# Performance work log

Hardware: AMD Instinct MI355X
Metric: run time of the kernel (lower is better)

The kernel has to match this reference:

```python
import jax, jax.numpy as jnp
import numpy as np

M = 16                      # multiplicity of each irrep block
INV3 = 1.0 / np.sqrt(3.0)   # w3j(1,1,0) component-normalized
INV2 = 1.0 / np.sqrt(2.0)   # w3j(1,1,1) component-normalized
A0 = 1.0 / np.sqrt(2.0 * M) # fan-in norm for 0e outputs (2 paths x mul 16)
A1 = 1.0 / np.sqrt(3.0 * M) # fan-in norm for 1o outputs (3 paths x mul 16)


def setup_inputs() -> dict:
    E, N, ED, HID = 100000, 10000, 32, 128
    WNUM = 2 * M * (2 * M) + 3 * M * M  # 1792 per-edge TP weights
    ks = jax.random.split(jax.random.key(0), 10)
    return {
        "dst": jax.random.randint(ks[0], (E,), 0, N),
        "x_src": jax.random.normal(ks[1], (E, 4 * M), jnp.float32),   # 16x0e+16x1o
        "x_dst": jax.random.normal(ks[2], (N, 4 * M), jnp.float32),
        "sh": jax.random.normal(ks[3], (E, 4), jnp.float32),          # 1x0e+1x1o
        "edge_attr": jax.random.normal(ks[4], (E, ED), jnp.float32),
        "We1": jax.random.normal(ks[5], (ED, HID), jnp.float32) / np.sqrt(ED),
        "be1": jnp.zeros((HID,), jnp.float32),
        "We2": jax.random.normal(ks[6], (HID, WNUM), jnp.float32) / np.sqrt(HID),
        "be2": jnp.zeros((WNUM,), jnp.float32),
        "Wr0": jax.random.normal(ks[7], (M, 2 * M), jnp.float32),     # 16x0e -> 32x0e
        "Wr1": jax.random.normal(ks[8], (M, M), jnp.float32),         # 16x1o -> 16x1o
    }


def _forward(dst, x_src, x_dst, sh, edge_attr, We1, be1, We2, be2, Wr0, Wr1):
    E = x_src.shape[0]
    N = x_dst.shape[0]
    o0 = 2 * M  # 32x0e tp output (scalars + gates)

    # edge MLP -> per-edge tensor-product weights [E, 1792]
    w = jax.nn.relu(edge_attr @ We1 + be1) @ We2 + be2
    i = 0
    w_ss = w[:, i:i + M * o0].reshape(E, M, o0); i += M * o0   # 0e x 0e -> 0e
    w_vv0 = w[:, i:i + M * o0].reshape(E, M, o0); i += M * o0  # 1o x 1o -> 0e
    w_sv = w[:, i:i + M * M].reshape(E, M, M); i += M * M      # 0e x 1o -> 1o
    w_vs = w[:, i:i + M * M].reshape(E, M, M); i += M * M      # 1o x 0e -> 1o
    w_vv1 = w[:, i:i + M * M].reshape(E, M, M)                 # 1o x 1o -> 1o

    s1 = x_src[:, :M]                       # [E, 16]
    v1 = x_src[:, M:].reshape(E, M, 3)      # [E, 16, 3]
    s2 = sh[:, 0]                           # [E]
    v2 = sh[:, 1:4]                         # [E, 3]

    # fully-connected tensor product with per-edge weights
    out0 = A0 * (jnp.einsum('em,emo->eo', s1 * s2[:, None], w_ss)
                 + INV3 * jnp.einsum('emc,ec,emo->eo', v1, v2, w_vv0))  # [E, 32]
    cross = jnp.cross(v1, v2[:, None, :])   # [E, 16, 3]
    out1 = A1 * (jnp.einsum('em,ec,emo->eoc', s1, v2, w_sv)
                 + jnp.einsum('emc,e,emo->eoc', v1, s2, w_vs)
                 + INV2 * jnp.einsum('emc,emo->eoc', cross, w_vv1))     # [E, 16, 3]
    msg = jnp.concatenate([out0, out1.reshape(E, -1)], axis=1)          # [E, 80]

    # scatter-mean over destination nodes
    ssum = jax.ops.segment_sum(msg, dst, num_segments=N)
    cnt = jax.ops.segment_sum(jnp.ones((E,), msg.dtype), dst, num_segments=N)
    msg = ssum / jnp.maximum(cnt, 1.0)[:, None]                          # [N, 80]

    # residual equivariant linear on x_dst
    sd = x_dst[:, :M]
    vd = x_dst[:, M:].reshape(N, M, 3)
    res0 = (sd @ Wr0) / np.sqrt(M)                                       # [N, 32]
    res1 = jnp.einsum('nmc,mo->noc', vd, Wr1) / np.sqrt(M)               # [N, 16, 3]
    msg = msg + jnp.concatenate([res0, res1.reshape(N, -1)], axis=1)

    # gate nonlinearity: relu(scalars), sigmoid(gates) * gated vectors
    scalars = jax.nn.relu(msg[:, :M])
    gates = jax.nn.sigmoid(msg[:, M:2 * M])
    gated = msg[:, 2 * M:].reshape(N, M, 3) * gates[:, :, None]
    return jnp.concatenate([scalars, gated.reshape(N, -1)], axis=1)      # [N, 64]


def reference(dst, x_src, x_dst, sh, edge_attr, We1, be1, We2, be2, Wr0, Wr1):
    return _forward(dst, x_src, x_dst, sh, edge_attr, We1, be1, We2, be2, Wr0, Wr1)
```

## Files before the change

### kernel.cpp

```cpp
#include <hip/hip_runtime.h>
#include <math.h>

#define WNUM 1792
#define HID 128

#define INV3C 0.5773502691896258f
#define INV2C 0.7071067811865476f
#define A0C   0.17677669529663687f
#define A1C   0.14433756729740643f
#define MAXDEG 64

typedef short bf8 __attribute__((ext_vector_type(8)));
typedef _Float16 f16x8 __attribute__((ext_vector_type(8)));
typedef _Float16 f16x4 __attribute__((ext_vector_type(4)));
typedef float f32x4 __attribute__((ext_vector_type(4)));

__device__ inline unsigned short f2bf(float f) {
  union { float f; unsigned u; } v; v.f = f;
  unsigned r = v.u + 0x7FFFu + ((v.u >> 16) & 1u);
  return (unsigned short)(r >> 16);
}
__device__ inline float bf2f(unsigned short h) {
  union { unsigned u; float f; } v; v.u = ((unsigned)h) << 16;
  return v.f;
}
__device__ inline float wscale(int t) {
  if (t < 32) return A0C;
  if (t < 64) return A0C * INV3C;
  if (t < 96) return A1C;
  return A1C * INV2C;
}

__global__ __launch_bounds__(256) void prep_kernel(
    const float* __restrict__ We1, const float* __restrict__ We2,
    const float* __restrict__ be2,
    unsigned short* __restrict__ we1x, _Float16* __restrict__ we2h,
    float* __restrict__ be2p, int* __restrict__ cntp, int N)
{
  int i = blockIdx.x * 256 + threadIdx.x;
  if (i < 28672) {
    int t = i >> 8, c = (i >> 6) & 3, lane = i & 63;
    int quad = lane >> 4, l15 = lane & 15;
    int col = t * 16 + l15;
    float sc = wscale(t);
    f16x8 v;
    #pragma unroll
    for (int j = 0; j < 8; ++j) {
      int k = c * 32 + quad * 8 + j;
      v[j] = (_Float16)(We2[(size_t)k * WNUM + col] * sc);
    }
    *(f16x8*)(we2h + (size_t)t * 2048 + c * 512 + lane * 8) = v;
  } else if (i < 29184) {
    int q = i - 28672;
    int c1 = q >> 6, lane = q & 63;
    int quad = lane >> 4, l15 = lane & 15;
    int col = c1 * 16 + l15;
    bf8 hh, ll;
    #pragma unroll
    for (int j = 0; j < 8; ++j) {
      int k = quad * 8 + j;
      float v = We1[k * HID + col];
      unsigned short hi = f2bf(v);
      hh[j] = (short)hi;
      ll[j] = (short)f2bf(v - bf2f(hi));
    }
    *(bf8*)(we1x + c1 * 1024 + lane * 8) = hh;
    *(bf8*)(we1x + c1 * 1024 + 512 + lane * 8) = ll;
  } else if (i < 30976) {
    int q = i - 29184;
    int t = q >> 4, l16 = q & 15;
    be2p[(t >> 1) * 32 + l16 * 2 + (t & 1)] = be2[q] * wscale(t);
  } else if (i < 30976 + N) {
    cntp[i - 30976] = 0;
  }
}

__device__ inline void chains2(const f16x8* a0, const f16x8* a1,
    f16x8 b0, f16x8 b1, f16x8 b2, f16x8 b3,
    f16x8 b4, f16x8 b5, f16x8 b6, f16x8 b7,
    float2 bias, f32x4* wa, f32x4* wb)
{
  f32x4 ca0 = {bias.x, bias.x, bias.x, bias.x};
  f32x4 cb0 = {bias.y, bias.y, bias.y, bias.y};
  f32x4 ca1 = ca0, cb1 = cb0;
  ca0 = __builtin_amdgcn_mfma_f32_16x16x32_f16(a0[0], b0, ca0, 0, 0, 0);
  cb0 = __builtin_amdgcn_mfma_f32_16x16x32_f16(a0[0], b4, cb0, 0, 0, 0);
  ca1 = __builtin_amdgcn_mfma_f32_16x16x32_f16(a1[0], b0, ca1, 0, 0, 0);
  cb1 = __builtin_amdgcn_mfma_f32_16x16x32_f16(a1[0], b4, cb1, 0, 0, 0);
  ca0 = __builtin_amdgcn_mfma_f32_16x16x32_f16(a0[1], b1, ca0, 0, 0, 0);
  cb0 = __builtin_amdgcn_mfma_f32_16x16x32_f16(a0[1], b5, cb0, 0, 0, 0);
  ca1 = __builtin_amdgcn_mfma_f32_16x16x32_f16(a1[1], b1, ca1, 0, 0, 0);
  cb1 = __builtin_amdgcn_mfma_f32_16x16x32_f16(a1[1], b5, cb1, 0, 0, 0);
  ca0 = __builtin_amdgcn_mfma_f32_16x16x32_f16(a0[2], b2, ca0, 0, 0, 0);
  cb0 = __builtin_amdgcn_mfma_f32_16x16x32_f16(a0[2], b6, cb0, 0, 0, 0);
  ca1 = __builtin_amdgcn_mfma_f32_16x16x32_f16(a1[2], b2, ca1, 0, 0, 0);
  cb1 = __builtin_amdgcn_mfma_f32_16x16x32_f16(a1[2], b6, cb1, 0, 0, 0);
  ca0 = __builtin_amdgcn_mfma_f32_16x16x32_f16(a0[3], b3, ca0, 0, 0, 0);
  cb0 = __builtin_amdgcn_mfma_f32_16x16x32_f16(a0[3], b7, cb0, 0, 0, 0);
  ca1 = __builtin_amdgcn_mfma_f32_16x16x32_f16(a1[3], b3, ca1, 0, 0, 0);
  cb1 = __builtin_amdgcn_mfma_f32_16x16x32_f16(a1[3], b7, cb1, 0, 0, 0);
  wa[0] = ca0; wb[0] = cb0; wa[1] = ca1; wb[1] = cb1;
}

__device__ inline void pair_mm(const _Float16* __restrict__ bG, const float* bp, int p,
                               const f16x8 (&af)[2][4], f32x4* wa, f32x4* wb)
{
  f16x8 b0 = *(const f16x8*)(bG);
  f16x8 b1 = *(const f16x8*)(bG + 512);
  f16x8 b2 = *(const f16x8*)(bG + 1024);
  f16x8 b3 = *(const f16x8*)(bG + 1536);
  f16x8 b4 = *(const f16x8*)(bG + 2048);
  f16x8 b5 = *(const f16x8*)(bG + 2560);
  f16x8 b6 = *(const f16x8*)(bG + 3072);
  f16x8 b7 = *(const f16x8*)(bG + 3584);
  float2 bias2 = *(const float2*)(bp + p * 32);
  chains2(af[0], af[1], b0, b1, b2, b3, b4, b5, b6, b7, bias2, wa, wb);
}

template <bool MSG>
__global__ __launch_bounds__(256, 2) void edge_kernel(
    const float* __restrict__ ea, const float* __restrict__ xsrc,
    const float* __restrict__ sh, const int* __restrict__ dst,
    const float* __restrict__ be1,
    const unsigned short* __restrict__ we1x, const _Float16* __restrict__ we2h,
    const float* __restrict__ be2p,
    float* __restrict__ outp, int* __restrict__ eidx, int* __restrict__ cntp, int E)
{
  const int lane = threadIdx.x & 63;
  const int w    = threadIdx.x >> 6;
  const int quad = lane >> 4;
  const int l16  = lane & 15;
  const int eb   = (blockIdx.x * 4 + w) * 32;

  __shared__ _Float16 h_s[4][16][136];
  __shared__ _Float16 s1h_s[4][16][32];
  __shared__ _Float16 v1h_s[4][16][3][32];
  __shared__ float4 vq_s[4][32];

  if (lane < 32) {
    int ge = eb + lane;
    if (ge < E) {
      int node = dst[ge];
      int pos = atomicAdd(cntp + node, 1);
      if (MSG) { if (pos < MAXDEG) eidx[node * MAXDEG + pos] = ge; }
    }
  }

  {
    int e2 = lane >> 1, mg = lane & 1;
    int ge = eb + e2;
    if (ge < E) {
      const float* xp = xsrc + (size_t)ge * 64;
      float4 sq0 = *(const float4*)(xp + mg * 8);
      float4 sq1 = *(const float4*)(xp + mg * 8 + 4);
      float s1a[8] = {sq0.x,sq0.y,sq0.z,sq0.w,sq1.x,sq1.y,sq1.z,sq1.w};
      const float* vp = xp + 16 + mg * 24;
      float la[24];
      #pragma unroll
      for (int qv = 0; qv < 6; ++qv) {
        float4 t = *(const float4*)(vp + qv * 4);
        la[qv*4+0] = t.x; la[qv*4+1] = t.y; la[qv*4+2] = t.z; la[qv*4+3] = t.w;
      }
      float4 shq = *(const float4*)(sh + (size_t)ge * 4);
      float s2 = shq.x, v2x = shq.y, v2y = shq.z, v2z = shq.w;
      #pragma unroll
      for (int mi = 0; mi < 8; ++mi) {
        int m = mg * 8 + mi;
        float v1x = la[mi*3], v1y = la[mi*3+1], v1z = la[mi*3+2];
        s1h_s[w][m][e2] = (_Float16)s1a[mi];
        v1h_s[w][m][0][e2] = (_Float16)v1x;
        v1h_s[w][m][1][e2] = (_Float16)v1y;
        v1h_s[w][m][2][e2] = (_Float16)v1z;
      }
      if (mg == 0) vq_s[w][e2] = make_float4(v2x, v2y, v2z, s2);
    } else {
      #pragma unroll
      for (int mi = 0; mi < 8; ++mi) {
        int m = mg * 8 + mi;
        s1h_s[w][m][e2] = (_Float16)0.f;
        v1h_s[w][m][0][e2] = (_Float16)0.f;
        v1h_s[w][m][1][e2] = (_Float16)0.f;
        v1h_s[w][m][2][e2] = (_Float16)0.f;
      }
      if (mg == 0) vq_s[w][e2] = make_float4(0,0,0,0);
    }
  }

  f16x8 af[2][4];
  {
    const unsigned short* wb1 = we1x + lane * 8;
    #pragma unroll
    for (int g = 0; g < 2; ++g) {
      bf8 ah, al;
      {
        int gea = eb + g * 16 + l16; if (gea > E - 1) gea = E - 1;
        const float* ep = ea + (size_t)gea * 32 + quad * 8;
        float4 p0 = *(const float4*)ep;
        float4 p1 = *(const float4*)(ep + 4);
        float pv[8] = {p0.x,p0.y,p0.z,p0.w,p1.x,p1.y,p1.z,p1.w};
        #pragma unroll
        for (int j = 0; j < 8; ++j) {
          unsigned short hi = f2bf(pv[j]);
          ah[j] = (short)hi;
          al[j] = (short)f2bf(pv[j] - bf2f(hi));
        }
      }
      #pragma unroll 2
      for (int c = 0; c < 8; ++c) {
        bf8 bh = *(const bf8*)(wb1 + c * 1024);
        bf8 bl = *(const bf8*)(wb1 + c * 1024 + 512);
        float bias = be1[c * 16 + l16];
        f32x4 hc = {bias, bias, bias, bias};
        hc = __builtin_amdgcn_mfma_f32_16x16x32_bf16(al, bh, hc, 0, 0, 0);
        hc = __builtin_amdgcn_mfma_f32_16x16x32_bf16(ah, bl, hc, 0, 0, 0);
        hc = __builtin_amdgcn_mfma_f32_16x16x32_bf16(ah, bh, hc, 0, 0, 0);
        #pragma unroll
        for (int r = 0; r < 4; ++r)
          h_s[w][quad * 4 + r][c * 16 + l16] = (_Float16)fmaxf(hc[r], 0.f);
      }
      #pragma unroll
      for (int ch = 0; ch < 4; ++ch)
        af[g][ch] = *(const f16x8*)&h_s[w][l16][ch * 32 + quad * 8];
      asm volatile("s_waitcnt lgkmcnt(0)" ::: "memory");
      __builtin_amdgcn_sched_barrier(0);
    }
  }

  const float* bp = be2p + l16 * 2;
  const _Float16* bG0 = we2h + lane * 8;
  float m0a[2][4] = {{0,0,0,0},{0,0,0,0}}, m0b[2][4] = {{0,0,0,0},{0,0,0,0}};

  {
    float s2v[2][4];
    #pragma unroll
    for (int g = 0; g < 2; ++g)
      #pragma unroll
      for (int r = 0; r < 4; ++r)
        s2v[g][r] = vq_s[w][g * 16 + quad * 4 + r].w;

    #pragma unroll 1
    for (int i = 0; i < 16; i += 2) {
      f32x4 wa[2], wb[2];
      pair_mm(bG0 + (size_t)i * 4096, bp, i, af, wa, wb);
      #pragma unroll
      for (int g = 0; g < 2; ++g) {
        f16x4 fv = *(const f16x4*)&s1h_s[w][i][g * 16 + quad * 4];
        #pragma unroll
        for (int r = 0; r < 4; ++r) {
          float f = (float)fv[r] * s2v[g][r];
          m0a[g][r] = fmaf(wa[g][r], f, m0a[g][r]);
          m0b[g][r] = fmaf(wb[g][r], f, m0b[g][r]);
        }
      }
      pair_mm(bG0 + (size_t)(i + 1) * 4096, bp, i + 1, af, wa, wb);
      #pragma unroll
      for (int g = 0; g < 2; ++g) {
        f16x4 fv = *(const f16x4*)&s1h_s[w][i + 1][g * 16 + quad * 4];
        #pragma unroll
        for (int r = 0; r < 4; ++r) {
          float f = (float)fv[r] * s2v[g][r];
          m0a[g][r] = fmaf(wa[g][r], f, m0a[g][r]);
          m0b[g][r] = fmaf(wb[g][r], f, m0b[g][r]);
        }
      }
    }
  }

  {
    float v2xv[2][4], v2yv[2][4], v2zv[2][4];
    #pragma unroll
    for (int g = 0; g < 2; ++g)
      #pragma unroll
      for (int r = 0; r < 4; ++r) {
        float4 q = vq_s[w][g * 16 + quad * 4 + r];
        v2xv[g][r] = q.x; v2yv[g][r] = q.y; v2zv[g][r] = q.z;
      }

    #pragma unroll 1
    for (int i = 0; i < 16; i += 2) {
      int pg = 16 + i;
      f32x4 wa[2], wb[2];
      pair_mm(bG0 + (size_t)pg * 4096, bp, pg, af, wa, wb);
      #pragma unroll
      for (int g = 0; g < 2; ++g) {
        f16x4 xA = *(const f16x4*)&v1h_s[w][i][0][g * 16 + quad * 4];
        f16x4 yA = *(const f16x4*)&v1h_s[w][i][1][g * 16 + quad * 4];
        f16x4 zA = *(const f16x4*)&v1h_s[w][i][2][g * 16 + quad * 4];
        #pragma unroll
        for (int r = 0; r < 4; ++r) {
          float f = fmaf((float)zA[r], v2zv[g][r],
                    fmaf((float)yA[r], v2yv[g][r], (float)xA[r] * v2xv[g][r]));
          m0a[g][r] = fmaf(wa[g][r], f, m0a[g][r]);
          m0b[g][r] = fmaf(wb[g][r], f, m0b[g][r]);
        }
      }
      pair_mm(bG0 + (size_t)(pg + 1) * 4096, bp, pg + 1, af, wa, wb);
      #pragma unroll
      for (int g = 0; g < 2; ++g) {
        f16x4 xA = *(const f16x4*)&v1h_s[w][i + 1][0][g * 16 + quad * 4];
        f16x4 yA = *(const f16x4*)&v1h_s[w][i + 1][1][g * 16 + quad * 4];
        f16x4 zA = *(const f16x4*)&v1h_s[w][i + 1][2][g * 16 + quad * 4];
        #pragma unroll
        for (int r = 0; r < 4; ++r) {
          float f = fmaf((float)zA[r], v2zv[g][r],
                    fmaf((float)yA[r], v2yv[g][r], (float)xA[r] * v2xv[g][r]));
          m0a[g][r] = fmaf(wa[g][r], f, m0a[g][r]);
          m0b[g][r] = fmaf(wb[g][r], f, m0b[g][r]);
        }
      }
    }
  }

  #pragma unroll
  for (int g = 0; g < 2; ++g)
    #pragma unroll
    for (int r = 0; r < 4; ++r) {
      int ge = eb + g * 16 + quad * 4 + r;
      if (ge < E) {
        if (MSG) {
          float* mp = outp + (size_t)ge * 80;
          mp[l16]      = m0a[g][r];
          mp[16 + l16] = m0b[g][r];
        } else {
          float* ap = outp + (size_t)dst[ge] * 80;
          atomicAdd(ap + l16,      m0a[g][r]);
          atomicAdd(ap + 16 + l16, m0b[g][r]);
        }
      }
    }

  float sg[2][4] = {{0,0,0,0},{0,0,0,0}};
  #pragma unroll 1
  for (int i = 0; i < 8; i += 2) {
    int pg = 32 + i;
    f32x4 wa[2], wb[2];
    pair_mm(bG0 + (size_t)pg * 4096, bp, pg, af, wa, wb);
    #pragma unroll
    for (int g = 0; g < 2; ++g) {
      f16x4 sA = *(const f16x4*)&s1h_s[w][2*i][g * 16 + quad * 4];
      f16x4 sB = *(const f16x4*)&s1h_s[w][2*i + 1][g * 16 + quad * 4];
      #pragma unroll
      for (int r = 0; r < 4; ++r)
        sg[g][r] = fmaf(wb[g][r], (float)sB[r], fmaf(wa[g][r], (float)sA[r], sg[g][r]));
    }
    pair_mm(bG0 + (size_t)(pg + 1) * 4096, bp, pg + 1, af, wa, wb);
    #pragma unroll
    for (int g = 0; g < 2; ++g) {
      f16x4 sA = *(const f16x4*)&s1h_s[w][2*i + 2][g * 16 + quad * 4];
      f16x4 sB = *(const f16x4*)&s1h_s[w][2*i + 3][g * 16 + quad * 4];
      #pragma unroll
      for (int r = 0; r < 4; ++r)
        sg[g][r] = fmaf(wb[g][r], (float)sB[r], fmaf(wa[g][r], (float)sA[r], sg[g][r]));
    }
  }
  float4 vq[2][4];
  #pragma unroll
  for (int g = 0; g < 2; ++g)
    #pragma unroll
    for (int r = 0; r < 4; ++r) vq[g][r] = vq_s[w][g * 16 + quad * 4 + r];

  float m1x[2][4], m1y[2][4], m1z[2][4];
  #pragma unroll
  for (int g = 0; g < 2; ++g)
    #pragma unroll
    for (int r = 0; r < 4; ++r) {
      m1x[g][r] = sg[g][r] * vq[g][r].x;
      m1y[g][r] = sg[g][r] * vq[g][r].y;
      m1z[g][r] = sg[g][r] * vq[g][r].z;
    }

  #pragma unroll
  for (int sec = 0; sec < 2; ++sec) {
    float ux[2][4] = {{0,0,0,0},{0,0,0,0}}, uy[2][4] = {{0,0,0,0},{0,0,0,0}},
          uz[2][4] = {{0,0,0,0},{0,0,0,0}};
    int base = 40 + sec * 8;
    #pragma unroll 1
    for (int i = 0; i < 8; i += 2) {
      int pg = base + i;
      f32x4 wa[2], wb[2];
      pair_mm(bG0 + (size_t)pg * 4096, bp, pg, af, wa, wb);
      #pragma unroll
      for (int g = 0; g < 2; ++g) {
        f16x4 xA = *(const f16x4*)&v1h_s[w][2*i][0][g*16 + quad*4];
        f16x4 xB = *(const f16x4*)&v1h_s[w][2*i+1][0][g*16 + quad*4];
        f16x4 yA = *(const f16x4*)&v1h_s[w][2*i][1][g*16 + quad*4];
        f16x4 yB = *(const f16x4*)&v1h_s[w][2*i+1][1][g*16 + quad*4];
        f16x4 zA = *(const f16x4*)&v1h_s[w][2*i][2][g*16 + quad*4];
        f16x4 zB = *(const f16x4*)&v1h_s[w][2*i+1][2][g*16 + quad*4];
        #pragma unroll
        for (int r = 0; r < 4; ++r) {
          ux[g][r] = fmaf(wb[g][r], (float)xB[r], fmaf(wa[g][r], (float)xA[r], ux[g][r]));
          uy[g][r] = fmaf(wb[g][r], (float)yB[r], fmaf(wa[g][r], (float)yA[r], uy[g][r]));
          uz[g][r] = fmaf(wb[g][r], (float)zB[r], fmaf(wa[g][r], (float)zA[r], uz[g][r]));
        }
      }
      pair_mm(bG0 + (size_t)(pg + 1) * 4096, bp, pg + 1, af, wa, wb);
      #pragma unroll
      for (int g = 0; g < 2; ++g) {
        f16x4 xA = *(const f16x4*)&v1h_s[w][2*i+2][0][g*16 + quad*4];
        f16x4 xB = *(const f16x4*)&v1h_s[w][2*i+3][0][g*16 + quad*4];
        f16x4 yA = *(const f16x4*)&v1h_s[w][2*i+2][1][g*16 + quad*4];
        f16x4 yB = *(const f16x4*)&v1h_s[w][2*i+3][1][g*16 + quad*4];
        f16x4 zA = *(const f16x4*)&v1h_s[w][2*i+2][2][g*16 + quad*4];
        f16x4 zB = *(const f16x4*)&v1h_s[w][2*i+3][2][g*16 + quad*4];
        #pragma unroll
        for (int r = 0; r < 4; ++r) {
          ux[g][r] = fmaf(wb[g][r], (float)xB[r], fmaf(wa[g][r], (float)xA[r], ux[g][r]));
          uy[g][r] = fmaf(wb[g][r], (float)yB[r], fmaf(wa[g][r], (float)yA[r], uy[g][r]));
          uz[g][r] = fmaf(wb[g][r], (float)zB[r], fmaf(wa[g][r], (float)zA[r], uz[g][r]));
        }
      }
    }
    if (sec == 0) {
      #pragma unroll
      for (int g = 0; g < 2; ++g)
        #pragma unroll
        for (int r = 0; r < 4; ++r) {
          m1x[g][r] = fmaf(vq[g][r].w, ux[g][r], m1x[g][r]);
          m1y[g][r] = fmaf(vq[g][r].w, uy[g][r], m1y[g][r]);
          m1z[g][r] = fmaf(vq[g][r].w, uz[g][r], m1z[g][r]);
        }
    } else {
      #pragma unroll
      for (int g = 0; g < 2; ++g)
        #pragma unroll
        for (int r = 0; r < 4; ++r) {
          m1x[g][r] = fmaf(uy[g][r], vq[g][r].z, m1x[g][r]);
          m1x[g][r] = fmaf(-uz[g][r], vq[g][r].y, m1x[g][r]);
          m1y[g][r] = fmaf(uz[g][r], vq[g][r].x, m1y[g][r]);
          m1y[g][r] = fmaf(-ux[g][r], vq[g][r].z, m1y[g][r]);
          m1z[g][r] = fmaf(ux[g][r], vq[g][r].y, m1z[g][r]);
          m1z[g][r] = fmaf(-uy[g][r], vq[g][r].x, m1z[g][r]);
        }
    }
  }

  #pragma unroll
  for (int g = 0; g < 2; ++g)
    #pragma unroll
    for (int r = 0; r < 4; ++r) {
      int ge = eb + g * 16 + quad * 4 + r;
      if (ge < E) {
        if (MSG) {
          float* mp = outp + (size_t)ge * 80;
          mp[32 + l16*3 + 0] = m1x[g][r];
          mp[32 + l16*3 + 1] = m1y[g][r];
          mp[32 + l16*3 + 2] = m1z[g][r];
        } else {
          float* ap = outp + (size_t)dst[ge] * 80;
          atomicAdd(ap + 32 + l16*3 + 0, m1x[g][r]);
          atomicAdd(ap + 32 + l16*3 + 1, m1y[g][r]);
          atomicAdd(ap + 32 + l16*3 + 2, m1z[g][r]);
        }
      }
    }
}

__global__ __launch_bounds__(128) void node_gather_kernel(
    const float* __restrict__ msg, const int* __restrict__ eidx,
    const int* __restrict__ cntp,
    const float* __restrict__ xdst, const float* __restrict__ Wr0,
    const float* __restrict__ Wr1, float* __restrict__ out, int N)
{
  int n = blockIdx.x;
  if (n >= N) return;
  int j = threadIdx.x;
  int c0 = cntp[n];
  int deg = c0 < MAXDEG ? c0 : MAXDEG;
  float inv = 1.0f / fmaxf((float)c0, 1.0f);
  __shared__ float s_sum[80];
  if (j < 80) {
    float s = 0.f;
    const int* ep = eidx + (size_t)n * MAXDEG;
    int i = 0;
    for (; i + 1 < deg; i += 2) {
      int e0 = ep[i], e1 = ep[i + 1];
      s += msg[(size_t)e0 * 80 + j] + msg[(size_t)e1 * 80 + j];
    }
    if (i < deg) s += msg[(size_t)ep[i] * 80 + j];
    s_sum[j] = s * inv;
  }
  __syncthreads();
  if (j >= 64) return;
  const float* xd = xdst + (size_t)n * 64;
  float* op = out + (size_t)n * 64;
  if (j < 16) {
    float s = 0.f;
    #pragma unroll
    for (int m = 0; m < 16; ++m) s = fmaf(xd[m], Wr0[m * 32 + j], s);
    op[j] = fmaxf(s_sum[j] + 0.25f * s, 0.f);
  } else {
    int jj = j - 16;
    int o = (jj * 86) >> 8;
    int c = jj - o * 3;
    float tg = 0.f, v = 0.f;
    #pragma unroll
    for (int m = 0; m < 16; ++m) {
      tg = fmaf(xd[m], Wr0[m * 32 + 16 + o], tg);
      v  = fmaf(xd[16 + m * 3 + c], Wr1[m * 16 + o], v);
    }
    float g = 1.0f / (1.0f + expf(-(s_sum[16 + o] + 0.25f * tg)));
    op[16 + jj] = (s_sum[32 + jj] + 0.25f * v) * g;
  }
}

__global__ __launch_bounds__(256) void node_kernel(
    const float* __restrict__ accn, const int* __restrict__ cntp,
    const float* __restrict__ xdst, const float* __restrict__ Wr0,
    const float* __restrict__ Wr1, float* __restrict__ out, int N)
{
  int idx = blockIdx.x * 256 + threadIdx.x;
  int n = idx >> 6, j = idx & 63;
  if (n >= N) return;
  float inv = 1.0f / fmaxf((float)cntp[n], 1.0f);
  const float* ap = accn + (size_t)n * 80;
  const float* xd = xdst + (size_t)n * 64;
  float* op = out + (size_t)n * 64;
  if (j < 16) {
    float s = 0.f;
    #pragma unroll
    for (int m = 0; m < 16; ++m) s = fmaf(xd[m], Wr0[m * 32 + j], s);
    op[j] = fmaxf(ap[j] * inv + 0.25f * s, 0.f);
  } else {
    int jj = j - 16;
    int o = (jj * 86) >> 8;
    int c = jj - o * 3;
    float tg = 0.f, v = 0.f;
    #pragma unroll
    for (int m = 0; m < 16; ++m) {
      tg = fmaf(xd[m], Wr0[m * 32 + 16 + o], tg);
      v  = fmaf(xd[16 + m * 3 + c], Wr1[m * 16 + o], v);
    }
    float g = 1.0f / (1.0f + expf(-(ap[16 + o] * inv + 0.25f * tg)));
    op[16 + jj] = (ap[32 + jj] * inv + 0.25f * v) * g;
  }
}

extern "C" void kernel_launch(void* const* d_in, const int* in_sizes, int n_in,
                              void* d_out, int out_size, void* d_ws, size_t ws_size,
                              hipStream_t stream)
{
  const int*   dst  = (const int*)d_in[0];
  const float* xsrc = (const float*)d_in[1];
  const float* xdst = (const float*)d_in[2];
  const float* sh   = (const float*)d_in[3];
  const float* ea   = (const float*)d_in[4];
  const float* We1  = (const float*)d_in[5];
  const float* be1  = (const float*)d_in[6];
  const float* We2  = (const float*)d_in[7];
  const float* be2  = (const float*)d_in[8];
  const float* Wr0  = (const float*)d_in[9];
  const float* Wr1  = (const float*)d_in[10];
  const int E = in_sizes[0];
  const int N = in_sizes[2] / 64;

  char* ws = (char*)d_ws;
  _Float16* we2h = (_Float16*)ws;
  unsigned short* we1x = (unsigned short*)(ws + 458752);
  float* be2p = (float*)(ws + 475136);
  int*   cntp = (int*)(ws + 482560);
  size_t off = 482560 + (size_t)N * 4;
  off = (off + 15) & ~(size_t)15;

  size_t need_msg = off + (size_t)N * MAXDEG * 4 + (size_t)E * 80 * 4;
  bool use_msg = (ws_size >= need_msg);

  prep_kernel<<<(30976 + N + 255) / 256, 256, 0, stream>>>(We1, We2, be2,
      we1x, we2h, be2p, cntp, N);

  if (use_msg) {
    int* eidx = (int*)(ws + off);
    float* msg = (float*)(ws + off + (size_t)N * MAXDEG * 4);
    edge_kernel<true><<<(E + 127) / 128, 256, 0, stream>>>(ea, xsrc, sh, dst, be1,
        we1x, we2h, be2p, msg, eidx, cntp, E);
    node_gather_kernel<<<N, 128, 0, stream>>>(msg, eidx, cntp, xdst, Wr0, Wr1,
        (float*)d_out, N);
  } else {
    float* accn = (float*)(ws + off);
    hipMemsetAsync(accn, 0, (size_t)N * 320, stream);
    edge_kernel<false><<<(E + 127) / 128, 256, 0, stream>>>(ea, xsrc, sh, dst, be1,
        we1x, we2h, be2p, accn, (int*)nullptr, cntp, E);
    node_kernel<<<((size_t)N * 64 + 255) / 256, 256, 0, stream>>>(accn, cntp,
        xdst, Wr0, Wr1, (float*)d_out, N);
  }
}
```

Before: 201.0 us.

## Stream edge-MLP second-layer weights through LDS with double-buffered async loads

The second-layer weight tiles, previously read straight from global memory into registers, are now staged per wave into a double-buffered LDS region (shared with the hidden-activation buffer) using global_load_lds. The load for tile t+2 is issued while tile t is computed, with explicit vmcnt/lgkmcnt waits. The per-edge loops are restructured to process one 16-column tile at a time, bias is staged in LDS as fp16, and spherical-harmonic values are read from global memory instead of a shared staging array. This is meant to hide global load latency behind the MFMA work, at the cost of manual wait management and fp16 rounding of the bias.

```diff
diff --git a/kernel.cpp b/kernel.cpp
--- a/kernel.cpp
+++ b/kernel.cpp
@@ -73,48 +73,6 @@
   } else if (i < 30976 + N) {
     cntp[i - 30976] = 0;
   }
-}
-
-__device__ inline void chains2(const f16x8* a0, const f16x8* a1,
-    f16x8 b0, f16x8 b1, f16x8 b2, f16x8 b3,
-    f16x8 b4, f16x8 b5, f16x8 b6, f16x8 b7,
-    float2 bias, f32x4* wa, f32x4* wb)
-{
-  f32x4 ca0 = {bias.x, bias.x, bias.x, bias.x};
-  f32x4 cb0 = {bias.y, bias.y, bias.y, bias.y};
-  f32x4 ca1 = ca0, cb1 = cb0;
-  ca0 = __builtin_amdgcn_mfma_f32_16x16x32_f16(a0[0], b0, ca0, 0, 0, 0);
-  cb0 = __builtin_amdgcn_mfma_f32_16x16x32_f16(a0[0], b4, cb0, 0, 0, 0);
-  ca1 = __builtin_amdgcn_mfma_f32_16x16x32_f16(a1[0], b0, ca1, 0, 0, 0);
-  cb1 = __builtin_amdgcn_mfma_f32_16x16x32_f16(a1[0], b4, cb1, 0, 0, 0);
-  ca0 = __builtin_amdgcn_mfma_f32_16x16x32_f16(a0[1], b1, ca0, 0, 0, 0);
-  cb0 = __builtin_amdgcn_mfma_f32_16x16x32_f16(a0[1], b5, cb0, 0, 0, 0);
-  ca1 = __builtin_amdgcn_mfma_f32_16x16x32_f16(a1[1], b1, ca1, 0, 0, 0);
-  cb1 = __builtin_amdgcn_mfma_f32_16x16x32_f16(a1[1], b5, cb1, 0, 0, 0);
-  ca0 = __builtin_amdgcn_mfma_f32_16x16x32_f16(a0[2], b2, ca0, 0, 0, 0);
-  cb0 = __builtin_amdgcn_mfma_f32_16x16x32_f16(a0[2], b6, cb0, 0, 0, 0);
-  ca1 = __builtin_amdgcn_mfma_f32_16x16x32_f16(a1[2], b2, ca1, 0, 0, 0);
-  cb1 = __builtin_amdgcn_mfma_f32_16x16x32_f16(a1[2], b6, cb1, 0, 0, 0);
-  ca0 = __builtin_amdgcn_mfma_f32_16x16x32_f16(a0[3], b3, ca0, 0, 0, 0);
-  cb0 = __builtin_amdgcn_mfma_f32_16x16x32_f16(a0[3], b7, cb0, 0, 0, 0);
-  ca1 = __builtin_amdgcn_mfma_f32_16x16x32_f16(a1[3], b3, ca1, 0, 0, 0);
-  cb1 = __builtin_amdgcn_mfma_f32_16x16x32_f16(a1[3], b7, cb1, 0, 0, 0);
-  wa[0] = ca0; wb[0] = cb0; wa[1] = ca1; wb[1] = cb1;
-}
-
-__device__ inline void pair_mm(const _Float16* __restrict__ bG, const float* bp, int p,
-                               const f16x8 (&af)[2][4], f32x4* wa, f32x4* wb)
-{
-  f16x8 b0 = *(const f16x8*)(bG);
-  f16x8 b1 = *(const f16x8*)(bG + 512);
-  f16x8 b2 = *(const f16x8*)(bG + 1024);
-  f16x8 b3 = *(const f16x8*)(bG + 1536);
-  f16x8 b4 = *(const f16x8*)(bG + 2048);
-  f16x8 b5 = *(const f16x8*)(bG + 2560);
-  f16x8 b6 = *(const f16x8*)(bG + 3072);
-  f16x8 b7 = *(const f16x8*)(bG + 3584);
-  float2 bias2 = *(const float2*)(bp + p * 32);
-  chains2(af[0], af[1], b0, b1, b2, b3, b4, b5, b6, b7, bias2, wa, wb);
 }
 
 template <bool MSG>
@@ -132,10 +90,51 @@
   const int l16  = lane & 15;
   const int eb   = (blockIdx.x * 4 + w) * 32;
 
-  __shared__ _Float16 h_s[4][16][136];
+  __shared__ union WaveMem {
+    _Float16 h[16][136];
+    _Float16 B[2][2048];
+  } uw[4];
   __shared__ _Float16 s1h_s[4][16][32];
   __shared__ _Float16 v1h_s[4][16][3][32];
-  __shared__ float4 vq_s[4][32];
+  __shared__ _Float16 biasL[1792];
+
+  #define STAGE_H(h_) { \
+    const _Float16* gsrc_ = we2h + (size_t)(h_) * 2048; \
+    _Float16* ldst_ = &uw[w].B[(h_) & 1][0]; \
+    _Pragma("unroll") \
+    for (int k_ = 0; k_ < 4; ++k_) \
+      __builtin_amdgcn_global_load_lds( \
+        (const __attribute__((address_space(1))) void*)(gsrc_ + k_ * 512 + lane * 8), \
+        (__attribute__((address_space(3))) void*)(ldst_ + k_ * 512), 16, 0, 0); \
+  }
+  #define FENCE_LGKM { asm volatile("s_waitcnt lgkmcnt(0)" ::: "memory"); \
+                       __builtin_amdgcn_sched_barrier(0); }
+  #define FENCE_VM4  { asm volatile("s_waitcnt vmcnt(4)" ::: "memory"); \
+                       __builtin_amdgcn_sched_barrier(0); }
+  #define FENCE_VM0  { asm volatile("s_waitcnt vmcnt(0)" ::: "memory"); \
+                       __builtin_amdgcn_sched_barrier(0); }
+
+  #define TILE(t_, ...) { \
+    const _Float16* bL_ = &uw[w].B[(t_) & 1][lane * 8]; \
+    f16x8 b0_ = *(const f16x8*)(bL_); \
+    f16x8 b1_ = *(const f16x8*)(bL_ + 512); \
+    f16x8 b2_ = *(const f16x8*)(bL_ + 1024); \
+    f16x8 b3_ = *(const f16x8*)(bL_ + 1536); \
+    float bs_ = (float)biasL[((t_) >> 1) * 32 + l16 * 2 + ((t_) & 1)]; \
+    FENCE_LGKM \
+    if ((t_) + 2 < 112) { STAGE_H((t_) + 2) __builtin_amdgcn_sched_barrier(0); } \
+    f32x4 w0 = {bs_, bs_, bs_, bs_}, w1 = w0; \
+    w0 = __builtin_amdgcn_mfma_f32_16x16x32_f16(af[0][0], b0_, w0, 0, 0, 0); \
+    w1 = __builtin_amdgcn_mfma_f32_16x16x32_f16(af[1][0], b0_, w1, 0, 0, 0); \
+    w0 = __builtin_amdgcn_mfma_f32_16x16x32_f16(af[0][1], b1_, w0, 0, 0, 0); \
+    w1 = __builtin_amdgcn_mfma_f32_16x16x32_f16(af[1][1], b1_, w1, 0, 0, 0); \
+    w0 = __builtin_amdgcn_mfma_f32_16x16x32_f16(af[0][2], b2_, w0, 0, 0, 0); \
+    w1 = __builtin_amdgcn_mfma_f32_16x16x32_f16(af[1][2], b2_, w1, 0, 0, 0); \
+    w0 = __builtin_amdgcn_mfma_f32_16x16x32_f16(af[0][3], b3_, w0, 0, 0, 0); \
+    w1 = __builtin_amdgcn_mfma_f32_16x16x32_f16(af[1][3], b3_, w1, 0, 0, 0); \
+    { __VA_ARGS__ } \
+    if ((t_) + 2 < 112) { FENCE_VM4 } else { FENCE_VM0 } \
+  }
 
   if (lane < 32) {
     int ge = eb + lane;
@@ -144,6 +143,13 @@
       int pos = atomicAdd(cntp + node, 1);
       if (MSG) { if (pos < MAXDEG) eidx[node * MAXDEG + pos] = ge; }
     }
+  }
+
+  {
+    int base = lane * 28;
+    #pragma unroll
+    for (int k = 0; k < 28; ++k)
+      biasL[base + k] = (_Float16)be2p[base + k];
   }
 
   {
@@ -161,18 +167,14 @@
         float4 t = *(const float4*)(vp + qv * 4);
         la[qv*4+0] = t.x; la[qv*4+1] = t.y; la[qv*4+2] = t.z; la[qv*4+3] = t.w;
       }
-      float4 shq = *(const float4*)(sh + (size_t)ge * 4);
-      float s2 = shq.x, v2x = shq.y, v2y = shq.z, v2z = shq.w;
       #pragma unroll
       for (int mi = 0; mi < 8; ++mi) {
         int m = mg * 8 + mi;
-        float v1x = la[mi*3], v1y = la[mi*3+1], v1z = la[mi*3+2];
         s1h_s[w][m][e2] = (_Float16)s1a[mi];
-        v1h_s[w][m][0][e2] = (_Float16)v1x;
-        v1h_s[w][m][1][e2] = (_Float16)v1y;
-        v1h_s[w][m][2][e2] = (_Float16)v1z;
-      }
-      if (mg == 0) vq_s[w][e2] = make_float4(v2x, v2y, v2z, s2);
+        v1h_s[w][m][0][e2] = (_Float16)la[mi*3];
+        v1h_s[w][m][1][e2] = (_Float16)la[mi*3+1];
+        v1h_s[w][m][2][e2] = (_Float16)la[mi*3+2];
+      }
     } else {
       #pragma unroll
       for (int mi = 0; mi < 8; ++mi) {
@@ -182,7 +184,6 @@
         v1h_s[w][m][1][e2] = (_Float16)0.f;
         v1h_s[w][m][2][e2] = (_Float16)0.f;
       }
-      if (mg == 0) vq_s[w][e2] = make_float4(0,0,0,0);
     }
   }
 
@@ -216,54 +217,53 @@
         hc = __builtin_amdgcn_mfma_f32_16x16x32_bf16(ah, bh, hc, 0, 0, 0);
         #pragma unroll
         for (int r = 0; r < 4; ++r)
-          h_s[w][quad * 4 + r][c * 16 + l16] = (_Float16)fmaxf(hc[r], 0.f);
+          uw[w].h[quad * 4 + r][c * 16 + l16] = (_Float16)fmaxf(hc[r], 0.f);
       }
       #pragma unroll
       for (int ch = 0; ch < 4; ++ch)
-        af[g][ch] = *(const f16x8*)&h_s[w][l16][ch * 32 + quad * 8];
-      asm volatile("s_waitcnt lgkmcnt(0)" ::: "memory");
-      __builtin_amdgcn_sched_barrier(0);
-    }
-  }
-
-  const float* bp = be2p + l16 * 2;
-  const _Float16* bG0 = we2h + lane * 8;
+        af[g][ch] = *(const f16x8*)&uw[w].h[l16][ch * 32 + quad * 8];
+      FENCE_LGKM
+    }
+  }
+
+  float s2v[2][4];
+  #pragma unroll
+  for (int g = 0; g < 2; ++g)
+    #pragma unroll
+    for (int r = 0; r < 4; ++r) {
+      int gev = eb + g * 16 + quad * 4 + r; if (gev > E - 1) gev = E - 1;
+      s2v[g][r] = sh[(size_t)gev * 4];
+    }
+
+  STAGE_H(0)
+  STAGE_H(1)
+  FENCE_VM4
+
   float m0a[2][4] = {{0,0,0,0},{0,0,0,0}}, m0b[2][4] = {{0,0,0,0},{0,0,0,0}};
 
-  {
-    float s2v[2][4];
-    #pragma unroll
-    for (int g = 0; g < 2; ++g)
-      #pragma unroll
-      for (int r = 0; r < 4; ++r)
-        s2v[g][r] = vq_s[w][g * 16 + quad * 4 + r].w;
-
-    #pragma unroll 1
-    for (int i = 0; i < 16; i += 2) {
-      f32x4 wa[2], wb[2];
-      pair_mm(bG0 + (size_t)i * 4096, bp, i, af, wa, wb);
-      #pragma unroll
-      for (int g = 0; g < 2; ++g) {
-        f16x4 fv = *(const f16x4*)&s1h_s[w][i][g * 16 + quad * 4];
-        #pragma unroll
-        for (int r = 0; r < 4; ++r) {
-          float f = (float)fv[r] * s2v[g][r];
-          m0a[g][r] = fmaf(wa[g][r], f, m0a[g][r]);
-          m0b[g][r] = fmaf(wb[g][r], f, m0b[g][r]);
-        }
-      }
-      pair_mm(bG0 + (size_t)(i + 1) * 4096, bp, i + 1, af, wa, wb);
-      #pragma unroll
-      for (int g = 0; g < 2; ++g) {
-        f16x4 fv = *(const f16x4*)&s1h_s[w][i + 1][g * 16 + quad * 4];
-        #pragma unroll
-        for (int r = 0; r < 4; ++r) {
-          float f = (float)fv[r] * s2v[g][r];
-          m0a[g][r] = fmaf(wa[g][r], f, m0a[g][r]);
-          m0b[g][r] = fmaf(wb[g][r], f, m0b[g][r]);
-        }
-      }
-    }
+  #pragma unroll 1
+  for (int i = 0; i < 16; ++i) {
+    float fA[4], fB[4];
+    {
+      f16x4 fv0 = *(const f16x4*)&s1h_s[w][i][quad * 4];
+      f16x4 fv1 = *(const f16x4*)&s1h_s[w][i][16 + quad * 4];
+      for (int r = 0; r < 4; ++r) {
+        fA[r] = (float)fv0[r] * s2v[0][r];
+        fB[r] = (float)fv1[r] * s2v[1][r];
+      }
+    }
+    TILE(2 * i,
+      for (int r = 0; r < 4; ++r) {
+        m0a[0][r] = fmaf(w0[r], fA[r], m0a[0][r]);
+        m0a[1][r] = fmaf(w1[r], fB[r], m0a[1][r]);
+      }
+    )
+    TILE(2 * i + 1,
+      for (int r = 0; r < 4; ++r) {
+        m0b[0][r] = fmaf(w0[r], fA[r], m0b[0][r]);
+        m0b[1][r] = fmaf(w1[r], fB[r], m0b[1][r]);
+      }
+    )
   }
 
   {
@@ -272,42 +272,40 @@
     for (int g = 0; g < 2; ++g)
       #pragma unroll
       for (int r = 0; r < 4; ++r) {
-        float4 q = vq_s[w][g * 16 + quad * 4 + r];
-        v2xv[g][r] = q.x; v2yv[g][r] = q.y; v2zv[g][r] = q.z;
+        int gev = eb + g * 16 + quad * 4 + r; if (gev > E - 1) gev = E - 1;
+        const float* sp = sh + (size_t)gev * 4;
+        v2xv[g][r] = sp[1]; v2yv[g][r] = sp[2]; v2zv[g][r] = sp[3];
       }
 
     #pragma unroll 1
-    for (int i = 0; i < 16; i += 2) {
-      int pg = 16 + i;
-      f32x4 wa[2], wb[2];
-      pair_mm(bG0 + (size_t)pg * 4096, bp, pg, af, wa, wb);
-      #pragma unroll
-      for (int g = 0; g < 2; ++g) {
-        f16x4 xA = *(const f16x4*)&v1h_s[w][i][0][g * 16 + quad * 4];
-        f16x4 yA = *(const f16x4*)&v1h_s[w][i][1][g * 16 + quad * 4];
-        f16x4 zA = *(const f16x4*)&v1h_s[w][i][2][g * 16 + quad * 4];
-        #pragma unroll
+    for (int i = 0; i < 16; ++i) {
+      float fA[4], fB[4];
+      {
+        f16x4 x0 = *(const f16x4*)&v1h_s[w][i][0][quad * 4];
+        f16x4 y0 = *(const f16x4*)&v1h_s[w][i][1][quad * 4];
+        f16x4 z0 = *(const f16x4*)&v1h_s[w][i][2][quad * 4];
+        f16x4 x1 = *(const f16x4*)&v1h_s[w][i][0][16 + quad * 4];
+        f16x4 y1 = *(const f16x4*)&v1h_s[w][i][1][16 + quad * 4];
+        f16x4 z1 = *(const f16x4*)&v1h_s[w][i][2][16 + quad * 4];
         for (int r = 0; r < 4; ++r) {
-          float f = fmaf((float)zA[r], v2zv[g][r],
-                    fmaf((float)yA[r], v2yv[g][r], (float)xA[r] * v2xv[g][r]));
-          m0a[g][r] = fmaf(wa[g][r], f, m0a[g][r]);
-          m0b[g][r] = fmaf(wb[g][r], f, m0b[g][r]);
-        }
-      }
-      pair_mm(bG0 + (size_t)(pg + 1) * 4096, bp, pg + 1, af, wa, wb);
-      #pragma unroll
-      for (int g = 0; g < 2; ++g) {
-        f16x4 xA = *(const f16x4*)&v1h_s[w][i + 1][0][g * 16 + quad * 4];
-        f16x4 yA = *(const f16x4*)&v1h_s[w][i + 1][1][g * 16 + quad * 4];
-        f16x4 zA = *(const f16x4*)&v1h_s[w][i + 1][2][g * 16 + quad * 4];
-        #pragma unroll
+          fA[r] = fmaf((float)z0[r], v2zv[0][r],
+                  fmaf((float)y0[r], v2yv[0][r], (float)x0[r] * v2xv[0][r]));
+          fB[r] = fmaf((float)z1[r], v2zv[1][r],
+                  fmaf((float)y1[r], v2yv[1][r], (float)x1[r] * v2xv[1][r]));
+        }
+      }
+      TILE(32 + 2 * i,
         for (int r = 0; r < 4; ++r) {
-          float f = fmaf((float)zA[r], v2zv[g][r],
-                    fmaf((float)yA[r], v2yv[g][r], (float)xA[r] * v2xv[g][r]));
-          m0a[g][r] = fmaf(wa[g][r], f, m0a[g][r]);
-          m0b[g][r] = fmaf(wb[g][r], f, m0b[g][r]);
-        }
-      }
+          m0a[0][r] = fmaf(w0[r], fA[r], m0a[0][r]);
+          m0a[1][r] = fmaf(w1[r], fB[r], m0a[1][r]);
+        }
+      )
+      TILE(33 + 2 * i,
+        for (int r = 0; r < 4; ++r) {
+          m0b[0][r] = fmaf(w0[r], fA[r], m0b[0][r]);
+          m0b[1][r] = fmaf(w1[r], fB[r], m0b[1][r]);
+        }
+      )
     }
   }
 
@@ -329,108 +327,82 @@
       }
     }
 
-  float sg[2][4] = {{0,0,0,0},{0,0,0,0}};
-  #pragma unroll 1
-  for (int i = 0; i < 8; i += 2) {
-    int pg = 32 + i;
-    f32x4 wa[2], wb[2];
-    pair_mm(bG0 + (size_t)pg * 4096, bp, pg, af, wa, wb);
-    #pragma unroll
-    for (int g = 0; g < 2; ++g) {
-      f16x4 sA = *(const f16x4*)&s1h_s[w][2*i][g * 16 + quad * 4];
-      f16x4 sB = *(const f16x4*)&s1h_s[w][2*i + 1][g * 16 + quad * 4];
-      #pragma unroll
-      for (int r = 0; r < 4; ++r)
-        sg[g][r] = fmaf(wb[g][r], (float)sB[r], fmaf(wa[g][r], (float)sA[r], sg[g][r]));
-    }
-    pair_mm(bG0 + (size_t)(pg + 1) * 4096, bp, pg + 1, af, wa, wb);
-    #pragma unroll
-    for (int g = 0; g < 2; ++g) {
-      f16x4 sA = *(const f16x4*)&s1h_s[w][2*i + 2][g * 16 + quad * 4];
-      f16x4 sB = *(const f16x4*)&s1h_s[w][2*i + 3][g * 16 + quad * 4];
-      #pragma unroll
-      for (int r = 0; r < 4; ++r)
-        sg[g][r] = fmaf(wb[g][r], (float)sB[r], fmaf(wa[g][r], (float)sA[r], sg[g][r]));
-    }
-  }
   float4 vq[2][4];
   #pragma unroll
   for (int g = 0; g < 2; ++g)
     #pragma unroll
-    for (int r = 0; r < 4; ++r) vq[g][r] = vq_s[w][g * 16 + quad * 4 + r];
+    for (int r = 0; r < 4; ++r) {
+      int gev = eb + g * 16 + quad * 4 + r; if (gev > E - 1) gev = E - 1;
+      vq[g][r] = *(const float4*)(sh + (size_t)gev * 4);
+    }
+
+  float sg[2][4] = {{0,0,0,0},{0,0,0,0}};
+  #pragma unroll 1
+  for (int ch = 0; ch < 16; ++ch) {
+    f16x4 s0 = *(const f16x4*)&s1h_s[w][ch][quad * 4];
+    f16x4 s1f = *(const f16x4*)&s1h_s[w][ch][16 + quad * 4];
+    TILE(64 + ch,
+      for (int r = 0; r < 4; ++r) {
+        sg[0][r] = fmaf(w0[r], (float)s0[r], sg[0][r]);
+        sg[1][r] = fmaf(w1[r], (float)s1f[r], sg[1][r]);
+      }
+    )
+  }
 
   float m1x[2][4], m1y[2][4], m1z[2][4];
   #pragma unroll
   for (int g = 0; g < 2; ++g)
     #pragma unroll
     for (int r = 0; r < 4; ++r) {
-      m1x[g][r] = sg[g][r] * vq[g][r].x;
-      m1y[g][r] = sg[g][r] * vq[g][r].y;
-      m1z[g][r] = sg[g][r] * vq[g][r].z;
+      m1x[g][r] = sg[g][r] * vq[g][r].y;
+      m1y[g][r] = sg[g][r] * vq[g][r].z;
+      m1z[g][r] = sg[g][r] * vq[g][r].w;
     }
 
   #pragma unroll
   for (int sec = 0; sec < 2; ++sec) {
     float ux[2][4] = {{0,0,0,0},{0,0,0,0}}, uy[2][4] = {{0,0,0,0},{0,0,0,0}},
           uz[2][4] = {{0,0,0,0},{0,0,0,0}};
-    int base = 40 + sec * 8;
+    int tb = 80 + sec * 16;
     #pragma unroll 1
-    for (int i = 0; i < 8; i += 2) {
-      int pg = base + i;
-      f32x4 wa[2], wb[2];
-      pair_mm(bG0 + (size_t)pg * 4096, bp, pg, af, wa, wb);
-      #pragma unroll
-      for (int g = 0; g < 2; ++g) {
-        f16x4 xA = *(const f16x4*)&v1h_s[w][2*i][0][g*16 + quad*4];
-        f16x4 xB = *(const f16x4*)&v1h_s[w][2*i+1][0][g*16 + quad*4];
-        f16x4 yA = *(const f16x4*)&v1h_s[w][2*i][1][g*16 + quad*4];
-        f16x4 yB = *(const f16x4*)&v1h_s[w][2*i+1][1][g*16 + quad*4];
-        f16x4 zA = *(const f16x4*)&v1h_s[w][2*i][2][g*16 + quad*4];
-        f16x4 zB = *(const f16x4*)&v1h_s[w][2*i+1][2][g*16 + quad*4];
-        #pragma unroll
+    for (int ch = 0; ch < 16; ++ch) {
+      f16x4 xA = *(const f16x4*)&v1h_s[w][ch][0][quad * 4];
+      f16x4 yA = *(const f16x4*)&v1h_s[w][ch][1][quad * 4];
+      f16x4 zA = *(const f16x4*)&v1h_s[w][ch][2][quad * 4];
+      f16x4 xB = *(const f16x4*)&v1h_s[w][ch][0][16 + quad * 4];
+      f16x4 yB = *(const f16x4*)&v1h_s[w][ch][1][16 + quad * 4];
+      f16x4 zB = *(const f16x4*)&v1h_s[w][ch][2][16 + quad * 4];
+      TILE(tb + ch,
         for (int r = 0; r < 4; ++r) {
-          ux[g][r] = fmaf(wb[g][r], (float)xB[r], fmaf(wa[g][r], (float)xA[r], ux[g][r]));
-          uy[g][r] = fmaf(wb[g][r], (float)yB[r], fmaf(wa[g][r], (float)yA[r], uy[g][r]));
-          uz[g][r] = fmaf(wb[g][r], (float)zB[r], fmaf(wa[g][r], (float)zA[r], uz[g][r]));
-        }
-      }
-      pair_mm(bG0 + (size_t)(pg + 1) * 4096, bp, pg + 1, af, wa, wb);
-      #pragma unroll
-      for (int g = 0; g < 2; ++g) {
-        f16x4 xA = *(const f16x4*)&v1h_s[w][2*i+2][0][g*16 + quad*4];
-        f16x4 xB = *(const f16x4*)&v1h_s[w][2*i+3][0][g*16 + quad*4];
-        f16x4 yA = *(const f16x4*)&v1h_s[w][2*i+2][1][g*16 + quad*4];
-        f16x4 yB = *(const f16x4*)&v1h_s[w][2*i+3][1][g*16 + quad*4];
-        f16x4 zA = *(const f16x4*)&v1h_s[w][2*i+2][2][g*16 + quad*4];
-        f16x4 zB = *(const f16x4*)&v1h_s[w][2*i+3][2][g*16 + quad*4];
-        #pragma unroll
-        for (int r = 0; r < 4; ++r) {
-          ux[g][r] = fmaf(wb[g][r], (float)xB[r], fmaf(wa[g][r], (float)xA[r], ux[g][r]));
-          uy[g][r] = fmaf(wb[g][r], (float)yB[r], fmaf(wa[g][r], (float)yA[r], uy[g][r]));
-          uz[g][r] = fmaf(wb[g][r], (float)zB[r], fmaf(wa[g][r], (float)zA[r], uz[g][r]));
-        }
-      }
+          ux[0][r] = fmaf(w0[r], (float)xA[r], ux[0][r]);
+          ux[1][r] = fmaf(w1[r], (float)xB[r], ux[1][r]);
+          uy[0][r] = fmaf(w0[r], (float)yA[r], uy[0][r]);
+          uy[1][r] = fmaf(w1[r], (float)yB[r], uy[1][r]);
+          uz[0][r] = fmaf(w0[r], (float)zA[r], uz[0][r]);
+          uz[1][r] = fmaf(w1[r], (float)zB[r], uz[1][r]);
+        }
+      )
     }
     if (sec == 0) {
       #pragma unroll
       for (int g = 0; g < 2; ++g)
         #pragma unroll
         for (int r = 0; r < 4; ++r) {
-          m1x[g][r] = fmaf(vq[g][r].w, ux[g][r], m1x[g][r]);
-          m1y[g][r] = fmaf(vq[g][r].w, uy[g][r], m1y[g][r]);
-          m1z[g][r] = fmaf(vq[g][r].w, uz[g][r], m1z[g][r]);
+          m1x[g][r] = fmaf(vq[g][r].x, ux[g][r], m1x[g][r]);
+          m1y[g][r] = fmaf(vq[g][r].x, uy[g][r], m1y[g][r]);
+          m1z[g][r] = fmaf(vq[g][r].x, uz[g][r], m1z[g][r]);
         }
     } else {
       #pragma unroll
       for (int g = 0; g < 2; ++g)
         #pragma unroll
         for (int r = 0; r < 4; ++r) {
-          m1x[g][r] = fmaf(uy[g][r], vq[g][r].z, m1x[g][r]);
-          m1x[g][r] = fmaf(-uz[g][r], vq[g][r].y, m1x[g][r]);
-          m1y[g][r] = fmaf(uz[g][r], vq[g][r].x, m1y[g][r]);
-          m1y[g][r] = fmaf(-ux[g][r], vq[g][r].z, m1y[g][r]);
-          m1z[g][r] = fmaf(ux[g][r], vq[g][r].y, m1z[g][r]);
-          m1z[g][r] = fmaf(-uy[g][r], vq[g][r].x, m1z[g][r]);
+          m1x[g][r] = fmaf(uy[g][r], vq[g][r].w, m1x[g][r]);
+          m1x[g][r] = fmaf(-uz[g][r], vq[g][r].z, m1x[g][r]);
+          m1y[g][r] = fmaf(uz[g][r], vq[g][r].y, m1y[g][r]);
+          m1y[g][r] = fmaf(-ux[g][r], vq[g][r].w, m1y[g][r]);
+          m1z[g][r] = fmaf(ux[g][r], vq[g][r].z, m1z[g][r]);
+          m1z[g][r] = fmaf(-uy[g][r], vq[g][r].y, m1z[g][r]);
         }
     }
   }
@@ -454,6 +426,11 @@
         }
       }
     }
+  #undef TILE
+  #undef STAGE_H
+  #undef FENCE_LGKM
+  #undef FENCE_VM4
+  #undef FENCE_VM0
 }
 
 __global__ __launch_bounds__(128) void node_gather_kernel(
```

Measured after the change: 207.1 us. 1.03x slower.
